# Performance work log

Measured on AMD Instinct MI355X. Metric: run time of the kernel, lower is better.

The kernel has to match this reference:

```python
import jax, jax.numpy as jnp
import numpy as np


def setup_inputs() -> dict:
    key = jax.random.key(0)
    ks = jax.random.split(key, 6)
    B, T, dim, H = 4, 4096, 2048, 16
    s = 0.02
    x = jax.random.normal(ks[0], (B, T, dim), jnp.float32)
    w_q = jax.random.normal(ks[1], (dim, dim), jnp.float32) * s
    w_k = jax.random.normal(ks[2], (dim, dim), jnp.float32) * s
    w_v = jax.random.normal(ks[3], (dim, dim), jnp.float32) * s
    w_o = jax.random.normal(ks[4], (dim, dim), jnp.float32) * s
    w_router = jax.random.normal(ks[5], (H, dim), jnp.float32) * s
    return {"x": x, "w_q": w_q, "w_k": w_k, "w_v": w_v, "w_o": w_o,
            "w_router": w_router, "top_k": 512}


def reference(x, w_q, w_k, w_v, w_o, w_router, top_k):
    B, T, dim = x.shape
    H = w_router.shape[0]
    hd = dim // H
    K = min(top_k, T)

    # router: per-head token scores [B, H, T] -> top-k indices [B, H, K]
    router_scores = jnp.einsum('btd,hd->bht', x, w_router)
    _, idx = jax.lax.top_k(router_scores, K)

    def proj(w):
        # [B, T, dim] -> [B, H, T, hd]
        return (x @ w.T).reshape(B, T, H, hd).transpose(0, 2, 1, 3)

    q, k, v = proj(w_q), proj(w_k), proj(w_v)

    gather = lambda t: jnp.take_along_axis(t, idx[..., None], axis=2)  # [B,H,K,hd]
    q_s, k_s, v_s = gather(q), gather(k), gather(v)

    scale = hd ** -0.5
    scores = jnp.einsum('bhkd,bhld->bhkl', q_s, k_s) * scale  # [B,H,K,K]
    # causal mask on ORIGINAL positions: query pos >= key pos
    can_attend = idx[..., :, None] >= idx[..., None, :]
    scores = jnp.where(can_attend, scores, -jnp.inf)
    attn = jax.nn.softmax(scores, axis=-1)
    out_s = jnp.einsum('bhkl,bhld->bhkd', attn, v_s)  # [B,H,K,hd]

    # scatter back into zeros at selected positions (indices unique per (b,h))
    out = jnp.zeros_like(q)
    bi = jnp.arange(B)[:, None, None]
    hi = jnp.arange(H)[None, :, None]
    out = out.at[bi, hi, idx].set(out_s)

    out = out.transpose(0, 2, 1, 3).reshape(B, T, dim)
    return out @ w_o.T
```

## Files before the change

### kernel.cpp

```cpp
#include <hip/hip_runtime.h>
#include <math.h>

#define BB 4
#define TT 4096
#define DD 2048
#define HH 16
#define HDIM 128
#define KSEL 512
#define NBH (BB*HH)

using short8  = __attribute__((ext_vector_type(8))) short;
using short4v = __attribute__((ext_vector_type(4))) short;
using f32x4   = __attribute__((ext_vector_type(4))) float;

__device__ __forceinline__ short f2bf(float f) {
  unsigned u = __float_as_uint(f);
  u += 0x7fffu + ((u >> 16) & 1u);
  return (short)(u >> 16);
}
__device__ __forceinline__ float bf2f(short s) {
  return __uint_as_float(((unsigned)(unsigned short)s) << 16);
}

__device__ __forceinline__ void gload16(const short* g, short* l) {
  __builtin_amdgcn_global_load_lds(
      (const __attribute__((address_space(1))) void*)g,
      (__attribute__((address_space(3))) void*)l, 16, 0, 0);
}

__global__ __launch_bounds__(256) void k_cvt_w(const float* __restrict__ wq,
    const float* __restrict__ wk, const float* __restrict__ wv,
    const float* __restrict__ wo, short* __restrict__ dst) {
  const int wsel = blockIdx.y;
  const float* s = (wsel == 0) ? wq : (wsel == 1) ? wk : (wsel == 2) ? wv : wo;
  size_t base = (size_t)blockIdx.x * 2048 + (size_t)threadIdx.x * 8;
  float4 a = *(const float4*)(s + base);
  float4 b = *(const float4*)(s + base + 4);
  short8 o;
  o[0] = f2bf(a.x); o[1] = f2bf(a.y); o[2] = f2bf(a.z); o[3] = f2bf(a.w);
  o[4] = f2bf(b.x); o[5] = f2bf(b.y); o[6] = f2bf(b.z); o[7] = f2bf(b.w);
  *(short8*)&dst[(size_t)wsel * 4194304 + base] = o;
}

__global__ __launch_bounds__(256) void k_router2(const float* __restrict__ x,
    const float* __restrict__ wr, float* __restrict__ part) {
  __shared__ __align__(16) float Xs[256][36];
  __shared__ __align__(16) float Ws[16][36];
  const int tb = blockIdx.x, kq = blockIdx.y;
  const int tid = threadIdx.x;
  const int row0 = tb * 256;
  const int tq = tid >> 2;
  const int hq = tid & 3;
  float acc[4][4];
#pragma unroll
  for (int i = 0; i < 4; ++i)
#pragma unroll
    for (int j = 0; j < 4; ++j) acc[i][j] = 0.f;
  const int srr = tid >> 3, scc = (tid & 7) * 4;
  for (int c = 0; c < 16; ++c) {
    const int k0 = kq * 512 + c * 32;
    __syncthreads();
    {
#pragma unroll
      for (int i = 0; i < 8; ++i) {
        int r = srr + i * 32;
        float4 v = *(const float4*)(x + (size_t)(row0 + r) * DD + k0 + scc);
        *(float4*)&Xs[r][scc] = v;
      }
      if (tid < 128) {
        float4 v = *(const float4*)(wr + (size_t)(tid >> 3) * DD + k0 + (tid & 7) * 4);
        *(float4*)&Ws[tid >> 3][(tid & 7) * 4] = v;
      }
    }
    __syncthreads();
#pragma unroll
    for (int k4 = 0; k4 < 8; ++k4) {
      float4 xv[4], wv[4];
#pragma unroll
      for (int i = 0; i < 4; ++i) xv[i] = *(const float4*)&Xs[tq + i * 64][k4 * 4];
#pragma unroll
      for (int j = 0; j < 4; ++j) wv[j] = *(const float4*)&Ws[hq + j * 4][k4 * 4];
#pragma unroll
      for (int i = 0; i < 4; ++i)
#pragma unroll
        for (int j = 0; j < 4; ++j)
          acc[i][j] += xv[i].x * wv[j].x + xv[i].y * wv[j].y +
                       xv[i].z * wv[j].z + xv[i].w * wv[j].w;
    }
  }
#pragma unroll
  for (int i = 0; i < 4; ++i) {
    int tg = row0 + tq + i * 64;
    int b = tg >> 12, t = tg & (TT - 1);
#pragma unroll
    for (int j = 0; j < 4; ++j)
      part[((size_t)kq * NBH + (b * HH + hq + j * 4)) * TT + t] = acc[i][j];
  }
}

__global__ __launch_bounds__(256) void k_router_sum(const float* __restrict__ part,
                                                    float* __restrict__ scores) {
  size_t i = ((size_t)blockIdx.x * 256 + threadIdx.x) * 4;
  const size_t S = (size_t)NBH * TT;
  float4 a = *(const float4*)(part + i);
  float4 b = *(const float4*)(part + S + i);
  float4 c = *(const float4*)(part + 2 * S + i);
  float4 d = *(const float4*)(part + 3 * S + i);
  float4 o = {((a.x + b.x) + c.x) + d.x, ((a.y + b.y) + c.y) + d.y,
              ((a.z + b.z) + c.z) + d.z, ((a.w + b.w) + c.w) + d.w};
  *(float4*)(scores + i) = o;
}

__global__ __launch_bounds__(512) void k_topk(const float* __restrict__ scores,
                                              int* __restrict__ idx,
                                              int* __restrict__ inv) {
  __shared__ unsigned hist[256];
  __shared__ unsigned ssum[257];
  __shared__ unsigned wtot[8];
  __shared__ unsigned sh_b;
  const int bh = blockIdx.x, tid = threadIdx.x;
  const int lane = tid & 63, wv = tid >> 6;
  const float* sc = scores + (size_t)bh * TT;
  unsigned key[8];
  {
    float4 v0 = *(const float4*)(sc + tid * 8);
    float4 v1 = *(const float4*)(sc + tid * 8 + 4);
    float vs[8] = {v0.x, v0.y, v0.z, v0.w, v1.x, v1.y, v1.z, v1.w};
#pragma unroll
    for (int i = 0; i < 8; ++i) {
      unsigned u = __float_as_uint(vs[i]);
      key[i] = (u & 0x80000000u) ? ~u : (u | 0x80000000u);
    }
  }
  unsigned prefix = 0, need = KSEL;
  for (int shift = 24; shift >= 0; shift -= 8) {
    if (tid < 256) hist[tid] = 0;
    __syncthreads();
#pragma unroll
    for (int i = 0; i < 8; ++i) {
      bool m = (shift == 24) || ((key[i] >> (shift + 8)) == prefix);
      if (m) atomicAdd(&hist[(key[i] >> shift) & 255], 1u);
    }
    __syncthreads();
    if (wv == 0) {
      unsigned v0 = hist[lane * 4], v1 = hist[lane * 4 + 1];
      unsigned v2 = hist[lane * 4 + 2], v3 = hist[lane * 4 + 3];
      unsigned s3 = v3, s2 = v2 + s3, s1 = v1 + s2, s0 = v0 + s1;
      unsigned t = s0;
#pragma unroll
      for (int off = 1; off < 64; off <<= 1) {
        unsigned o = __shfl_down(t, off);
        if (lane + off < 64) t += o;
      }
      unsigned above = t - s0;
      ssum[lane * 4]     = s0 + above;
      ssum[lane * 4 + 1] = s1 + above;
      ssum[lane * 4 + 2] = s2 + above;
      ssum[lane * 4 + 3] = s3 + above;
      if (lane == 0) ssum[256] = 0;
    }
    __syncthreads();
    if (tid < 256) {
      if (ssum[tid] >= need && ssum[tid + 1] < need) sh_b = (unsigned)tid;
    }
    __syncthreads();
    unsigned bstar = sh_b;
    need -= ssum[bstar + 1];
    prefix = (shift == 24) ? bstar : ((prefix << 8) | bstar);
  }
  const unsigned thr = prefix;
  unsigned cgt = 0, ceq = 0;
#pragma unroll
  for (int i = 0; i < 8; ++i) { cgt += (key[i] > thr); ceq += (key[i] == thr); }
  unsigned packed = (cgt << 16) | ceq;
  unsigned inc = packed;
#pragma unroll
  for (int off = 1; off < 64; off <<= 1) {
    unsigned o = __shfl_up(inc, off);
    if (lane >= off) inc += o;
  }
  if (lane == 63) wtot[wv] = inc;
  __syncthreads();
  unsigned wbase = 0;
#pragma unroll
  for (int w2 = 0; w2 < 8; ++w2) wbase += (w2 < wv) ? wtot[w2] : 0u;
  unsigned base = wbase + inc - packed;
  unsigned gt_before = base >> 16, eq_before = base & 0xffffu;
  int* op = idx + bh * KSEL;
  int* invrow = inv + (size_t)bh * TT;
#pragma unroll
  for (int i = 0; i < 8; ++i) {
    bool isgt = key[i] > thr, iseq = key[i] == thr;
    bool sel = isgt || (iseq && eq_before < need);
    int pos = -1;
    if (sel) {
      pos = (int)(gt_before + (eq_before < need ? eq_before : need));
      op[pos] = tid * 8 + i;
    }
    invrow[tid * 8 + i] = pos;
    gt_before += isgt; eq_before += iseq;
  }
}

__global__ __launch_bounds__(256, 2) void k_qkv_mfma(
    const float* __restrict__ x, const short* __restrict__ wqb,
    const short* __restrict__ wkb, const short* __restrict__ wvb,
    const int* __restrict__ idx,
    short* __restrict__ q_s, short* __restrict__ k_s, short* __restrict__ v_t) {
  __shared__ __align__(16) short As[64 * 64];
  __shared__ __align__(16) short Bs[3][128 * 64];
  __shared__ int tIdx[64];
  const int L = blockIdx.x;
  const int bh = (L & 7) * 8 + (L >> 6);
  const int rt = (L >> 3) & 7;
  const int b = bh >> 4, h = bh & 15;
  const int tid = threadIdx.x;
  if (tid < 64) tIdx[tid] = idx[bh * KSEL + rt * 64 + tid];
  __syncthreads();
  const int lane = tid & 63, w = tid >> 6;
  const int g = lane >> 4, r15 = lane & 15;
  const int arow = tid >> 2, kq = tid & 3;
  const int lcol8 = lane >> 3, lslot = lane & 7;
  const float* aPtr = x + ((size_t)b * TT + tIdx[arow]) * DD + kq * 16;
  f32x4 acc[4][6];
#pragma unroll
  for (int m = 0; m < 4; ++m)
#pragma unroll
    for (int n = 0; n < 6; ++n) acc[m][n] = (f32x4){0.f, 0.f, 0.f, 0.f};
  const int rm = arow & 7;
  for (int k0 = 0; k0 < DD; k0 += 64) {
    __syncthreads();
    {
      float4 a0 = *(const float4*)(aPtr + k0);
      float4 a1 = *(const float4*)(aPtr + k0 + 4);
      float4 a2 = *(const float4*)(aPtr + k0 + 8);
      float4 a3 = *(const float4*)(aPtr + k0 + 12);
      short8 p0, p1;
      p0[0] = f2bf(a0.x); p0[1] = f2bf(a0.y); p0[2] = f2bf(a0.z); p0[3] = f2bf(a0.w);
      p0[4] = f2bf(a1.x); p0[5] = f2bf(a1.y); p0[6] = f2bf(a1.z); p0[7] = f2bf(a1.w);
      p1[0] = f2bf(a2.x); p1[1] = f2bf(a2.y); p1[2] = f2bf(a2.z); p1[3] = f2bf(a2.w);
      p1[4] = f2bf(a3.x); p1[5] = f2bf(a3.y); p1[6] = f2bf(a3.z); p1[7] = f2bf(a3.w);
      *(short8*)&As[arow * 64 + ((2 * kq) ^ rm) * 8] = p0;
      *(short8*)&As[arow * 64 + ((2 * kq + 1) ^ rm) * 8] = p1;
#pragma unroll
      for (int t = 0; t < 12; ++t) {
        int gi = w * 12 + t;
        int p = gi >> 4;
        int c0 = (gi & 15) << 3;
        int col = c0 + lcol8;
        const short* wsrc = (p == 0 ? wqb : p == 1 ? wkb : wvb)
                          + ((size_t)(h * HDIM + col)) * DD + k0 + ((lslot ^ (col & 7)) << 3);
        gload16(wsrc, &Bs[p][c0 * 64]);
      }
    }
    __syncthreads();
#pragma unroll
    for (int ks = 0; ks < 2; ++ks) {
      short8 af[4], bfr[6];
#pragma unroll
      for (int m = 0; m < 4; ++m) {
        int row = m * 16 + r15;
        af[m] = *(const short8*)&As[row * 64 + ((ks * 4 + g) ^ (row & 7)) * 8];
      }
#pragma unroll
      for (int n = 0; n < 6; ++n) {
        int nf = w * 6 + n;
        int colr = (nf & 7) * 16 + r15;
        bfr[n] = *(const short8*)&Bs[nf >> 3][colr * 64 + ((ks * 4 + g) ^ (colr & 7)) * 8];
      }
#pragma unroll
      for (int m = 0; m < 4; ++m)
#pragma unroll
        for (int n = 0; n < 6; ++n)
          acc[m][n] = __builtin_amdgcn_mfma_f32_16x16x32_bf16(af[m], bfr[n], acc[m][n], 0, 0, 0);
    }
  }
#pragma unroll
  for (int n = 0; n < 6; ++n) {
    int nf = w * 6 + n;
    int p = nf >> 3;
    int col = (nf & 7) * 16 + r15;
    if (p == 2) {
#pragma unroll
      for (int m = 0; m < 4; ++m) {
        short4v pk;
#pragma unroll
        for (int r = 0; r < 4; ++r) pk[r] = f2bf(acc[m][n][r]);
        *(short4v*)&v_t[((size_t)bh * HDIM + col) * KSEL + rt * 64 + m * 16 + g * 4] = pk;
      }
    } else {
      short* dp = (p == 0) ? q_s : k_s;
#pragma unroll
      for (int m = 0; m < 4; ++m) {
        int row0 = rt * 64 + m * 16 + g * 4;
#pragma unroll
        for (int r = 0; r < 4; ++r)
          dp[((size_t)bh * KSEL + row0 + r) * HDIM + col] = f2bf(acc[m][n][r]);
      }
    }
  }
}

__global__ __launch_bounds__(256) void k_attn_mfma(const short* __restrict__ q_s,
    const short* __restrict__ k_s, const short* __restrict__ v_t,
    short* __restrict__ out_s) {
  __shared__ __align__(16) short Ks[64 * 128];
  __shared__ __align__(16) short Vt[128 * 64];
  __shared__ __align__(16) short Pl[4 * 16 * 72];
  const int bh = blockIdx.x, qt = blockIdx.y;
  const int tid = threadIdx.x;
  const int w = tid >> 6, lane = tid & 63;
  const int g = lane >> 4, r15 = lane & 15;
  const size_t bhbase = (size_t)bh * KSEL * HDIM;
  const int r0 = qt * 64;
  const float scale = 0.08838834764831845f;

  short8 qf[4];
  {
    const short* qrow = q_s + bhbase + (size_t)(r0 + w * 16 + r15) * HDIM;
#pragma unroll
    for (int ks = 0; ks < 4; ++ks)
      qf[ks] = *(const short8*)(qrow + ks * 32 + g * 8);
  }
  f32x4 o[8];
#pragma unroll
  for (int n = 0; n < 8; ++n) o[n] = (f32x4){0.f, 0.f, 0.f, 0.f};
  float mrow[4] = {-INFINITY, -INFINITY, -INFINITY, -INFINITY};
  float lrow[4] = {0.f, 0.f, 0.f, 0.f};

  short* myP = &Pl[w * 16 * 72];
  const int kl16 = lane >> 4, ks16 = lane & 15;
  const int vl8 = lane >> 3, vs8 = lane & 7;

  for (int kt = 0; kt <= qt; ++kt) {
    int l0 = kt * 64;
    __syncthreads();
    {
#pragma unroll
      for (int t = 0; t < 4; ++t) {
        int gi = w * 4 + t;
        int kr0 = gi * 4;
        int key = kr0 + kl16;
        const short* ksrc = k_s + bhbase + (size_t)(l0 + key) * HDIM + ((ks16 ^ (key & 7)) << 3);
        gload16(ksrc, &Ks[kr0 * 128]);
        int d0 = gi * 8;
        int d = d0 + vl8;
        const short* vsrc = v_t + ((size_t)bh * HDIM + d) * KSEL + l0 + ((vs8 ^ (d & 7)) << 3);
        gload16(vsrc, &Vt[d0 * 64]);
      }
    }
    __syncthreads();

    f32x4 s[4];
#pragma unroll
    for (int n = 0; n < 4; ++n) s[n] = (f32x4){0.f, 0.f, 0.f, 0.f};
#pragma unroll
    for (int ks = 0; ks < 4; ++ks) {
#pragma unroll
      for (int n = 0; n < 4; ++n) {
        int row = n * 16 + r15;
        short8 kf = *(const short8*)&Ks[row * 128 + ((ks * 4 + g) ^ (r15 & 7)) * 8];
        s[n] = __builtin_amdgcn_mfma_f32_16x16x32_bf16(qf[ks], kf, s[n], 0, 0, 0);
      }
    }

    const bool diag = (kt == qt);
    float sv[4][4];
#pragma unroll
    for (int n = 0; n < 4; ++n) {
      int key = kt * 64 + n * 16 + r15;
#pragma unroll
      for (int r = 0; r < 4; ++r) {
        float xv = s[n][r] * scale;
        int qrow = r0 + w * 16 + g * 4 + r;
        sv[n][r] = (diag && key > qrow) ? -INFINITY : xv;
      }
    }
    float corr[4];
#pragma unroll
    for (int r = 0; r < 4; ++r) {
      float tm = fmaxf(fmaxf(sv[0][r], sv[1][r]), fmaxf(sv[2][r], sv[3][r]));
#pragma unroll
      for (int off = 8; off; off >>= 1) tm = fmaxf(tm, __shfl_xor(tm, off));
      float newm = fmaxf(mrow[r], tm);
      corr[r] = __expf(mrow[r] - newm);
      mrow[r] = newm;
      float ps = 0.f;
#pragma unroll
      for (int n = 0; n < 4; ++n) {
        float pv = __expf(sv[n][r] - newm);
        sv[n][r] = pv;
        ps += pv;
      }
#pragma unroll
      for (int off = 8; off; off >>= 1) ps += __shfl_xor(ps, off);
      lrow[r] = lrow[r] * corr[r] + ps;
    }
    f32x4 corrv = {corr[0], corr[1], corr[2], corr[3]};
#pragma unroll
    for (int n = 0; n < 4; ++n)
#pragma unroll
      for (int r = 0; r < 4; ++r)
        myP[(g * 4 + r) * 72 + n * 16 + r15] = f2bf(sv[n][r]);
#pragma unroll
    for (int n = 0; n < 8; ++n) o[n] *= corrv;

    short8 pf[2];
#pragma unroll
    for (int ks = 0; ks < 2; ++ks)
      pf[ks] = *(const short8*)&myP[r15 * 72 + ks * 32 + g * 8];
#pragma unroll
    for (int ks = 0; ks < 2; ++ks)
#pragma unroll
      for (int n2 = 0; n2 < 8; ++n2) {
        int row = n2 * 16 + r15;
        short8 vf = *(const short8*)&Vt[row * 64 + ((ks * 4 + g) ^ (r15 & 7)) * 8];
        o[n2] = __builtin_amdgcn_mfma_f32_16x16x32_bf16(pf[ks], vf, o[n2], 0, 0, 0);
      }
  }

  float inv[4];
#pragma unroll
  for (int r = 0; r < 4; ++r) inv[r] = 1.f / lrow[r];
#pragma unroll
  for (int n2 = 0; n2 < 8; ++n2) {
#pragma unroll
    for (int r = 0; r < 4; ++r) {
      int qrow = r0 + w * 16 + g * 4 + r;
      out_s[bhbase + (size_t)qrow * HDIM + n2 * 16 + r15] = f2bf(o[n2][r] * inv[r]);
    }
  }
}

__global__ __launch_bounds__(256) void k_oproj_p1(
    const short* __restrict__ out_s_b, const short* __restrict__ wob,
    short* __restrict__ P) {
  __shared__ __align__(16) short As[128 * 64];
  __shared__ __align__(16) short Bs[128 * 64];
  const int h = blockIdx.x, rt = blockIdx.y, ct = blockIdx.z;
  const int tid = threadIdx.x;
  const int lane = tid & 63, wid = tid >> 6;
  const int wr = wid >> 1, wc = wid & 1;
  const int l8 = lane >> 3, s8 = lane & 7;
  f32x4 acc[4][4];
#pragma unroll
  for (int m = 0; m < 4; ++m)
#pragma unroll
    for (int n = 0; n < 4; ++n) acc[m][n] = (f32x4){0.f, 0.f, 0.f, 0.f};
  const int r15 = lane & 15, g = lane >> 4;
#pragma unroll
  for (int k0 = 0; k0 < HDIM; k0 += 64) {
    __syncthreads();
    {
#pragma unroll
      for (int t = 0; t < 4; ++t) {
        int gi = wid * 4 + t;
        int r0 = gi * 8;
        int row = r0 + l8;
        const short* asrc = out_s_b + ((size_t)h * KSEL + rt * 128 + row) * HDIM + k0
                          + ((s8 ^ (row & 7)) << 3);
        gload16(asrc, &As[r0 * 64]);
        const short* bsrc = wob + ((size_t)(ct * 128 + row)) * DD + h * HDIM + k0
                          + ((s8 ^ (row & 7)) << 3);
        gload16(bsrc, &Bs[r0 * 64]);
      }
    }
    __syncthreads();
#pragma unroll
    for (int ks = 0; ks < 2; ++ks) {
      short8 af[4], bfr[4];
#pragma unroll
      for (int m = 0; m < 4; ++m) {
        int row = wr * 64 + m * 16 + r15;
        int chunk = (ks * 4 + g) ^ (row & 7);
        af[m] = *(const short8*)&As[row * 64 + chunk * 8];
      }
#pragma unroll
      for (int n = 0; n < 4; ++n) {
        int col = wc * 64 + n * 16 + r15;
        int chunk = (ks * 4 + g) ^ (col & 7);
        bfr[n] = *(const short8*)&Bs[col * 64 + chunk * 8];
      }
#pragma unroll
      for (int m = 0; m < 4; ++m)
#pragma unroll
        for (int n = 0; n < 4; ++n)
          acc[m][n] = __builtin_amdgcn_mfma_f32_16x16x32_bf16(af[m], bfr[n], acc[m][n], 0, 0, 0);
    }
  }
#pragma unroll
  for (int m = 0; m < 4; ++m) {
#pragma unroll
    for (int r = 0; r < 4; ++r) {
      int row = rt * 128 + wr * 64 + m * 16 + g * 4 + r;
#pragma unroll
      for (int n = 0; n < 4; ++n) {
        int col = ct * 128 + wc * 64 + n * 16 + r15;
        P[((size_t)h * KSEL + row) * DD + col] = f2bf(acc[m][n][r]);
      }
    }
  }
}

__global__ __launch_bounds__(256) void k_oproj_p2(const short* __restrict__ P,
    const int* __restrict__ inv_b, float* __restrict__ out_b) {
  const int t = blockIdx.x, tid = threadIdx.x;
  const int c0 = tid * 8;
  float acc[8] = {0.f, 0.f, 0.f, 0.f, 0.f, 0.f, 0.f, 0.f};
#pragma unroll
  for (int h = 0; h < HH; ++h) {
    int k = inv_b[h * TT + t];
    if (k >= 0) {
      short8 pv = *(const short8*)&P[((size_t)h * KSEL + k) * DD + c0];
#pragma unroll
      for (int e = 0; e < 8; ++e) acc[e] += bf2f(pv[e]);
    }
  }
  float4 o0 = {acc[0], acc[1], acc[2], acc[3]};
  float4 o1 = {acc[4], acc[5], acc[6], acc[7]};
  *(float4*)&out_b[(size_t)t * DD + c0] = o0;
  *(float4*)&out_b[(size_t)t * DD + c0 + 4] = o1;
}

extern "C" void kernel_launch(void* const* d_in, const int* in_sizes, int n_in,
                              void* d_out, int out_size, void* d_ws, size_t ws_size,
                              hipStream_t stream) {
  (void)in_sizes; (void)n_in; (void)out_size; (void)ws_size;
  const float* x  = (const float*)d_in[0];
  const float* wq = (const float*)d_in[1];
  const float* wk = (const float*)d_in[2];
  const float* wv = (const float*)d_in[3];
  const float* wo = (const float*)d_in[4];
  const float* wr = (const float*)d_in[5];
  float* out = (float*)d_out;

  char* ws = (char*)d_ws;
  float* scores = (float*)ws;
  int*   idx    = (int*)(ws + 1048576);
  short* wqb    = (short*)(ws + 1179648);
  short* wkb    = wqb + 4194304;
  short* wvb    = wkb + 4194304;
  short* wob    = wvb + 4194304;
  short* out_s  = wob + 4194304;
  int*   inv    = (int*)((char*)out_s + 8388608);
  short* P      = (short*)((char*)inv + 1048576);
  short* q_s    = P;
  short* k_s    = P + 4194304;
  short* v_t    = P + 8388608;
  float* part   = (float*)P;

  k_cvt_w<<<dim3(2048, 4), 256, 0, stream>>>(wq, wk, wv, wo, wqb);
  k_router2<<<dim3(64, 4), 256, 0, stream>>>(x, wr, part);
  k_router_sum<<<256, 256, 0, stream>>>(part, scores);
  k_topk<<<NBH, 512, 0, stream>>>(scores, idx, inv);
  k_qkv_mfma<<<512, 256, 0, stream>>>(x, wqb, wkb, wvb, idx, q_s, k_s, v_t);
  k_attn_mfma<<<dim3(NBH, KSEL / 64), 256, 0, stream>>>(q_s, k_s, v_t, out_s);
  for (int b = 0; b < BB; ++b) {
    k_oproj_p1<<<dim3(HH, KSEL / 128, DD / 128), 256, 0, stream>>>(
        out_s + (size_t)b * HH * KSEL * HDIM, wob, P);
    k_oproj_p2<<<TT, 256, 0, stream>>>(
        P, inv + (size_t)b * HH * TT, out + (size_t)b * TT * DD);
  }
}
```

Baseline: 294.8 us.

## Emit bf16 copy of x in router pass and async-load it in QKV GEMM

The router kernel now also writes a bf16 copy of x while it streams x through shared memory, and uses a finer grid (128-row tiles, 8-way K split) with the partial-sum reducer widened to eight slices. When the workspace is large enough, the QKV projection kernel loads its gathered A rows directly from this bf16 buffer with asynchronous global-to-LDS loads instead of reading fp32 x and converting in registers. This halves the bytes gathered by the GEMM and removes the per-tile conversion work. In exchange the router pass writes an extra 64 MB and the reducer reads twice as many partial slices; a fallback path keeps the old behaviour for small workspaces.

```diff
diff --git a/kernel.cpp b/kernel.cpp
--- a/kernel.cpp
+++ b/kernel.cpp
@@ -43,53 +43,63 @@
 }
 
 __global__ __launch_bounds__(256) void k_router2(const float* __restrict__ x,
-    const float* __restrict__ wr, float* __restrict__ part) {
-  __shared__ __align__(16) float Xs[256][36];
+    const float* __restrict__ wr, float* __restrict__ part,
+    short* __restrict__ xb, const int writeXb) {
+  __shared__ __align__(16) float Xs[128][36];
   __shared__ __align__(16) float Ws[16][36];
   const int tb = blockIdx.x, kq = blockIdx.y;
   const int tid = threadIdx.x;
-  const int row0 = tb * 256;
-  const int tq = tid >> 2;
-  const int hq = tid & 3;
-  float acc[4][4];
-#pragma unroll
-  for (int i = 0; i < 4; ++i)
+  const int row0 = tb * 128;
+  const int tq = tid >> 2, hq = tid & 3;
+  float acc[2][4];
+#pragma unroll
+  for (int i = 0; i < 2; ++i)
 #pragma unroll
     for (int j = 0; j < 4; ++j) acc[i][j] = 0.f;
-  const int srr = tid >> 3, scc = (tid & 7) * 4;
-  for (int c = 0; c < 16; ++c) {
-    const int k0 = kq * 512 + c * 32;
+  const int sr = tid >> 1, sc = (tid & 1) * 16;
+  const float* xrow = x + (size_t)(row0 + sr) * DD + sc;
+  short* xbrow = xb + (size_t)(row0 + sr) * DD + sc;
+  for (int c = 0; c < 8; ++c) {
+    const int k0 = kq * 256 + c * 32;
     __syncthreads();
     {
-#pragma unroll
-      for (int i = 0; i < 8; ++i) {
-        int r = srr + i * 32;
-        float4 v = *(const float4*)(x + (size_t)(row0 + r) * DD + k0 + scc);
-        *(float4*)&Xs[r][scc] = v;
+      float4 v0 = *(const float4*)(xrow + k0);
+      float4 v1 = *(const float4*)(xrow + k0 + 4);
+      float4 v2 = *(const float4*)(xrow + k0 + 8);
+      float4 v3 = *(const float4*)(xrow + k0 + 12);
+      *(float4*)&Xs[sr][sc + 0]  = v0;
+      *(float4*)&Xs[sr][sc + 4]  = v1;
+      *(float4*)&Xs[sr][sc + 8]  = v2;
+      *(float4*)&Xs[sr][sc + 12] = v3;
+      if (writeXb) {
+        short8 b0, b1;
+        b0[0] = f2bf(v0.x); b0[1] = f2bf(v0.y); b0[2] = f2bf(v0.z); b0[3] = f2bf(v0.w);
+        b0[4] = f2bf(v1.x); b0[5] = f2bf(v1.y); b0[6] = f2bf(v1.z); b0[7] = f2bf(v1.w);
+        b1[0] = f2bf(v2.x); b1[1] = f2bf(v2.y); b1[2] = f2bf(v2.z); b1[3] = f2bf(v2.w);
+        b1[4] = f2bf(v3.x); b1[5] = f2bf(v3.y); b1[6] = f2bf(v3.z); b1[7] = f2bf(v3.w);
+        *(short8*)(xbrow + k0) = b0;
+        *(short8*)(xbrow + k0 + 8) = b1;
       }
       if (tid < 128) {
-        float4 v = *(const float4*)(wr + (size_t)(tid >> 3) * DD + k0 + (tid & 7) * 4);
-        *(float4*)&Ws[tid >> 3][(tid & 7) * 4] = v;
+        float4 wv4 = *(const float4*)(wr + (size_t)(tid >> 3) * DD + k0 + (tid & 7) * 4);
+        *(float4*)&Ws[tid >> 3][(tid & 7) * 4] = wv4;
       }
     }
     __syncthreads();
 #pragma unroll
     for (int k4 = 0; k4 < 8; ++k4) {
-      float4 xv[4], wv[4];
-#pragma unroll
-      for (int i = 0; i < 4; ++i) xv[i] = *(const float4*)&Xs[tq + i * 64][k4 * 4];
-#pragma unroll
-      for (int j = 0; j < 4; ++j) wv[j] = *(const float4*)&Ws[hq + j * 4][k4 * 4];
-#pragma unroll
-      for (int i = 0; i < 4; ++i)
-#pragma unroll
-        for (int j = 0; j < 4; ++j)
-          acc[i][j] += xv[i].x * wv[j].x + xv[i].y * wv[j].y +
-                       xv[i].z * wv[j].z + xv[i].w * wv[j].w;
-    }
-  }
-#pragma unroll
-  for (int i = 0; i < 4; ++i) {
+      float4 xv0 = *(const float4*)&Xs[tq][k4 * 4];
+      float4 xv1 = *(const float4*)&Xs[tq + 64][k4 * 4];
+#pragma unroll
+      for (int j = 0; j < 4; ++j) {
+        float4 wv4 = *(const float4*)&Ws[hq + j * 4][k4 * 4];
+        acc[0][j] += xv0.x * wv4.x + xv0.y * wv4.y + xv0.z * wv4.z + xv0.w * wv4.w;
+        acc[1][j] += xv1.x * wv4.x + xv1.y * wv4.y + xv1.z * wv4.z + xv1.w * wv4.w;
+      }
+    }
+  }
+#pragma unroll
+  for (int i = 0; i < 2; ++i) {
     int tg = row0 + tq + i * 64;
     int b = tg >> 12, t = tg & (TT - 1);
 #pragma unroll
@@ -102,13 +112,13 @@
                                                     float* __restrict__ scores) {
   size_t i = ((size_t)blockIdx.x * 256 + threadIdx.x) * 4;
   const size_t S = (size_t)NBH * TT;
-  float4 a = *(const float4*)(part + i);
-  float4 b = *(const float4*)(part + S + i);
-  float4 c = *(const float4*)(part + 2 * S + i);
-  float4 d = *(const float4*)(part + 3 * S + i);
-  float4 o = {((a.x + b.x) + c.x) + d.x, ((a.y + b.y) + c.y) + d.y,
-              ((a.z + b.z) + c.z) + d.z, ((a.w + b.w) + c.w) + d.w};
-  *(float4*)(scores + i) = o;
+  float4 s = *(const float4*)(part + i);
+#pragma unroll
+  for (int k = 1; k < 8; ++k) {
+    float4 v = *(const float4*)(part + k * S + i);
+    s.x += v.x; s.y += v.y; s.z += v.z; s.w += v.w;
+  }
+  *(float4*)(scores + i) = s;
 }
 
 __global__ __launch_bounds__(512) void k_topk(const float* __restrict__ scores,
@@ -202,10 +212,11 @@
   }
 }
 
+template <int AB>
 __global__ __launch_bounds__(256, 2) void k_qkv_mfma(
-    const float* __restrict__ x, const short* __restrict__ wqb,
-    const short* __restrict__ wkb, const short* __restrict__ wvb,
-    const int* __restrict__ idx,
+    const float* __restrict__ x, const short* __restrict__ xb,
+    const short* __restrict__ wqb, const short* __restrict__ wkb,
+    const short* __restrict__ wvb, const int* __restrict__ idx,
     short* __restrict__ q_s, short* __restrict__ k_s, short* __restrict__ v_t) {
   __shared__ __align__(16) short As[64 * 64];
   __shared__ __align__(16) short Bs[3][128 * 64];
@@ -219,29 +230,45 @@
   __syncthreads();
   const int lane = tid & 63, w = tid >> 6;
   const int g = lane >> 4, r15 = lane & 15;
-  const int arow = tid >> 2, kq = tid & 3;
   const int lcol8 = lane >> 3, lslot = lane & 7;
-  const float* aPtr = x + ((size_t)b * TT + tIdx[arow]) * DD + kq * 16;
+  const float* aPtr = nullptr;
+  const short* aSrc0 = nullptr; const short* aSrc1 = nullptr;
+  int arow = 0, rm = 0;
+  if constexpr (AB) {
+    int rowA0 = w * 16 + lcol8;
+    int rowA1 = rowA0 + 8;
+    aSrc0 = xb + ((size_t)b * TT + tIdx[rowA0]) * DD + ((lslot ^ lcol8) << 3);
+    aSrc1 = xb + ((size_t)b * TT + tIdx[rowA1]) * DD + ((lslot ^ lcol8) << 3);
+  } else {
+    arow = tid >> 2;
+    rm = arow & 7;
+    aPtr = x + ((size_t)b * TT + tIdx[arow]) * DD + (tid & 3) * 16;
+  }
   f32x4 acc[4][6];
 #pragma unroll
   for (int m = 0; m < 4; ++m)
 #pragma unroll
     for (int n = 0; n < 6; ++n) acc[m][n] = (f32x4){0.f, 0.f, 0.f, 0.f};
-  const int rm = arow & 7;
   for (int k0 = 0; k0 < DD; k0 += 64) {
     __syncthreads();
     {
-      float4 a0 = *(const float4*)(aPtr + k0);
-      float4 a1 = *(const float4*)(aPtr + k0 + 4);
-      float4 a2 = *(const float4*)(aPtr + k0 + 8);
-      float4 a3 = *(const float4*)(aPtr + k0 + 12);
-      short8 p0, p1;
-      p0[0] = f2bf(a0.x); p0[1] = f2bf(a0.y); p0[2] = f2bf(a0.z); p0[3] = f2bf(a0.w);
-      p0[4] = f2bf(a1.x); p0[5] = f2bf(a1.y); p0[6] = f2bf(a1.z); p0[7] = f2bf(a1.w);
-      p1[0] = f2bf(a2.x); p1[1] = f2bf(a2.y); p1[2] = f2bf(a2.z); p1[3] = f2bf(a2.w);
-      p1[4] = f2bf(a3.x); p1[5] = f2bf(a3.y); p1[6] = f2bf(a3.z); p1[7] = f2bf(a3.w);
-      *(short8*)&As[arow * 64 + ((2 * kq) ^ rm) * 8] = p0;
-      *(short8*)&As[arow * 64 + ((2 * kq + 1) ^ rm) * 8] = p1;
+      if constexpr (AB) {
+        gload16(aSrc0 + k0, &As[(w * 16) * 64]);
+        gload16(aSrc1 + k0, &As[(w * 16 + 8) * 64]);
+      } else {
+        float4 a0 = *(const float4*)(aPtr + k0);
+        float4 a1 = *(const float4*)(aPtr + k0 + 4);
+        float4 a2 = *(const float4*)(aPtr + k0 + 8);
+        float4 a3 = *(const float4*)(aPtr + k0 + 12);
+        short8 p0, p1;
+        p0[0] = f2bf(a0.x); p0[1] = f2bf(a0.y); p0[2] = f2bf(a0.z); p0[3] = f2bf(a0.w);
+        p0[4] = f2bf(a1.x); p0[5] = f2bf(a1.y); p0[6] = f2bf(a1.z); p0[7] = f2bf(a1.w);
+        p1[0] = f2bf(a2.x); p1[1] = f2bf(a2.y); p1[2] = f2bf(a2.z); p1[3] = f2bf(a2.w);
+        p1[4] = f2bf(a3.x); p1[5] = f2bf(a3.y); p1[6] = f2bf(a3.z); p1[7] = f2bf(a3.w);
+        int kq = tid & 3;
+        *(short8*)&As[arow * 64 + ((2 * kq) ^ rm) * 8] = p0;
+        *(short8*)&As[arow * 64 + ((2 * kq + 1) ^ rm) * 8] = p1;
+      }
 #pragma unroll
       for (int t = 0; t < 12; ++t) {
         int gi = w * 12 + t;
@@ -525,7 +552,7 @@
 extern "C" void kernel_launch(void* const* d_in, const int* in_sizes, int n_in,
                               void* d_out, int out_size, void* d_ws, size_t ws_size,
                               hipStream_t stream) {
-  (void)in_sizes; (void)n_in; (void)out_size; (void)ws_size;
+  (void)in_sizes; (void)n_in; (void)out_size;
   const float* x  = (const float*)d_in[0];
   const float* wq = (const float*)d_in[1];
   const float* wk = (const float*)d_in[2];
@@ -548,12 +575,18 @@
   short* k_s    = P + 4194304;
   short* v_t    = P + 8388608;
   float* part   = (float*)P;
+  const size_t NEED_XB = 144834560ULL;
+  const int big = (ws_size >= NEED_XB) ? 1 : 0;
+  short* xb = big ? (short*)(ws + 77725696) : (short*)ws;
 
   k_cvt_w<<<dim3(2048, 4), 256, 0, stream>>>(wq, wk, wv, wo, wqb);
-  k_router2<<<dim3(64, 4), 256, 0, stream>>>(x, wr, part);
+  k_router2<<<dim3(128, 8), 256, 0, stream>>>(x, wr, part, xb, big);
   k_router_sum<<<256, 256, 0, stream>>>(part, scores);
   k_topk<<<NBH, 512, 0, stream>>>(scores, idx, inv);
-  k_qkv_mfma<<<512, 256, 0, stream>>>(x, wqb, wkb, wvb, idx, q_s, k_s, v_t);
+  if (big)
+    k_qkv_mfma<1><<<512, 256, 0, stream>>>(x, xb, wqb, wkb, wvb, idx, q_s, k_s, v_t);
+  else
+    k_qkv_mfma<0><<<512, 256, 0, stream>>>(x, xb, wqb, wkb, wvb, idx, q_s, k_s, v_t);
   k_attn_mfma<<<dim3(NBH, KSEL / 64), 256, 0, stream>>>(q_s, k_s, v_t, out_s);
   for (int b = 0; b < BB; ++b) {
     k_oproj_p1<<<dim3(HH, KSEL / 128, DD / 128), 256, 0, stream>>>(
```

Result: no change. 299.3 us (+1.5%).
